# Kernel tuning notes

Measured on AMD Instinct MI355X. Metric: run time of the kernel, lower is better.

The kernel has to match this reference:

```python
import jax, jax.numpy as jnp
import numpy as np

NUM_HEADS = 16


def setup_inputs() -> dict:
    key = jax.random.key(0)
    ks = jax.random.split(key, 8)
    B, S, E = 2, 2048, 1024
    std = 0.02
    return {
        "q": jax.random.normal(ks[0], (B, S, E), dtype=jnp.float32),
        "k": jax.random.normal(ks[1], (B, S, E), dtype=jnp.float32),
        "v": jax.random.normal(ks[2], (B, S, E), dtype=jnp.float32),
        "Wq": jax.random.normal(ks[3], (E, E), dtype=jnp.float32) * std,
        "Wk": jax.random.normal(ks[4], (E, E), dtype=jnp.float32) * std,
        "Wv": jax.random.normal(ks[5], (E, E), dtype=jnp.float32) * std,
        "Wo": jax.random.normal(ks[6], (E, E), dtype=jnp.float32) * std,
        "bo": jnp.zeros((E,), dtype=jnp.float32),
    }


def reference(q, k, v, Wq, Wk, Wv, Wo, bo):
    B, S, E = q.shape
    H = NUM_HEADS
    D = E // H
    # projections (nn.Linear: x @ W.T)
    Q = (q @ Wq.T).reshape(B, S, H, D).transpose(0, 2, 1, 3)  # [B,H,S,D]
    K = (k @ Wk.T).reshape(B, S, H, D).transpose(0, 2, 1, 3)
    V = (v @ Wv.T).reshape(B, S, H, D).transpose(0, 2, 1, 3)
    scores = jnp.einsum("bhsd,bhtd->bhst", Q, K)  # [B,H,S,S]
    # causal mask applied before scaling (as in source; -inf/sqrt(d) == -inf)
    causal = jnp.tril(jnp.ones((S, S), dtype=bool))
    scores = jnp.where(causal, scores, -jnp.inf)
    scores = scores / np.sqrt(D).astype(np.float32)
    attn = jax.nn.softmax(scores, axis=-1)
    out = jnp.einsum("bhst,bhtd->bhsd", attn, V)  # [B,H,S,D]
    out = out.transpose(0, 2, 1, 3).reshape(B, S, E)
    return out @ Wo.T + bo
```

## Files before the change

kernel.cpp:

```cpp
#include <hip/hip_runtime.h>

typedef unsigned short u16;
typedef __bf16 bf16x8 __attribute__((ext_vector_type(8)));
typedef float f32x4 __attribute__((ext_vector_type(4)));
typedef unsigned u32x4 __attribute__((ext_vector_type(4)));

#define B_ 2
#define S_ 2048
#define E_ 1024
#define H_ 16
#define D_ 64
#define M_ (B_ * S_)

__device__ inline u16 f2bf(float f) {
  union { float f; unsigned int u; } c; c.f = f;
  unsigned int u = c.u;
  return (u16)((u + 0x7FFFu + ((u >> 16) & 1u)) >> 16);
}

__device__ inline f32x4 mfma16(bf16x8 a, bf16x8 b, f32x4 c) {
  return __builtin_amdgcn_mfma_f32_16x16x32_bf16(a, b, c, 0, 0, 0);
}

__device__ inline void gload16(const void* g, void* lds) {
  __builtin_amdgcn_global_load_lds(
      (const __attribute__((address_space(1))) unsigned int*)g,
      (__attribute__((address_space(3))) unsigned int*)lds, 16, 0, 0);
}

struct CvtArgs {
  const float* src[7];
  u16* dst[7];
  int n[7];
};

__global__ __launch_bounds__(256) void cvt_kernel(CvtArgs a) {
  const int arr = blockIdx.y;
  const int n = a.n[arr];
  const float* __restrict__ s = a.src[arr];
  u16* __restrict__ d = a.dst[arr];
  const int stride = gridDim.x * blockDim.x;
  for (int i = blockIdx.x * blockDim.x + threadIdx.x; i * 4 < n; i += stride) {
    const float4 f = *(const float4*)(s + 4 * i);
    ushort4 o;
    o.x = f2bf(f.x); o.y = f2bf(f.y); o.z = f2bf(f.z); o.w = f2bf(f.w);
    *(ushort4*)(d + 4 * i) = o;
  }
}

__global__ __launch_bounds__(256, 3) void qkv_gemm(
    const u16* __restrict__ qb, const u16* __restrict__ kb,
    const u16* __restrict__ vbp, const u16* __restrict__ Wqb,
    const u16* __restrict__ Wkb, const u16* __restrict__ Wvb,
    u16* __restrict__ Qh, u16* __restrict__ Kh, u16* __restrict__ Vt) {
  constexpr int BM = 128, BN = 128, BK = 32;
  __shared__ alignas(16) u16 As[3][BM * BK];
  __shared__ alignas(16) u16 Bs[3][BN * BK];

  const int wg = blockIdx.x;
  const int xcd = wg & 7, idx = wg >> 3;
  const int nb = idx & 7, mz = idx >> 3;
  const int z = mz >> 2;
  const int m0 = (xcd * 4 + (mz & 3)) * BM, n0 = nb * BN;

  const u16* A  = (z == 0) ? qb  : (z == 1) ? kb  : vbp;
  const u16* Bt = (z == 0) ? Wqb : (z == 1) ? Wkb : Wvb;
  u16* outp     = (z == 0) ? Qh  : (z == 1) ? Kh  : Vt;

  const int tid = threadIdx.x;
  const int wave = tid >> 6, lane = tid & 63;
  const int wm = (wave >> 1) * 64, wn = (wave & 1) * 64;
  const int fr = lane & 15, fc = lane >> 4;
  const int lrow = lane >> 2;
  const int lcol_sw = (((lane & 3) ^ ((lrow >> 1) & 3)) * 8);

  f32x4 acc[4][4] = {};

  u16 *aA = As[0], *aB = As[1], *aC = As[2];
  u16 *bA = Bs[0], *bB = Bs[1], *bC = Bs[2];

  auto stage = [&](int k0, u16* as, u16* bs) {
#pragma unroll
    for (int i = 0; i < 2; ++i) {
      const int chunk = wave * 2 + i;
      const int row = chunk * 16 + lrow;
      gload16(A + (size_t)(m0 + row) * E_ + k0 + lcol_sw, as + chunk * 16 * BK);
      gload16(Bt + (size_t)(n0 + row) * E_ + k0 + lcol_sw, bs + chunk * 16 * BK);
    }
  };

  constexpr int NK = E_ / BK;
  stage(0, aA, bA);
  stage(BK, aB, bB);

  const int sl = (fc ^ ((fr >> 1) & 3)) * 8;

  for (int t = 0; t < NK; ++t) {
    if (t + 1 < NK) {
      asm volatile("s_waitcnt vmcnt(4)" ::: "memory");
    } else {
      asm volatile("s_waitcnt vmcnt(0)" ::: "memory");
    }
    __builtin_amdgcn_s_barrier();
    __builtin_amdgcn_sched_barrier(0);

    if (t + 2 < NK) stage((t + 2) * BK, aC, bC);

    bf16x8 af[4], bfr[4];
#pragma unroll
    for (int mi = 0; mi < 4; ++mi)
      af[mi] = *(const bf16x8*)&aA[(wm + mi * 16 + fr) * BK + sl];
#pragma unroll
    for (int ni = 0; ni < 4; ++ni)
      bfr[ni] = *(const bf16x8*)&bA[(wn + ni * 16 + fr) * BK + sl];
    __builtin_amdgcn_s_setprio(1);
#pragma unroll
    for (int mi = 0; mi < 4; ++mi)
#pragma unroll
      for (int ni = 0; ni < 4; ++ni)
        acc[mi][ni] = mfma16(af[mi], bfr[ni], acc[mi][ni]);
    __builtin_amdgcn_s_setprio(0);

    u16* tp;
    tp = aA; aA = aB; aB = aC; aC = tp;
    tp = bA; bA = bB; bB = bC; bC = tp;
  }

#pragma unroll
  for (int mi = 0; mi < 4; ++mi)
#pragma unroll
    for (int ni = 0; ni < 4; ++ni)
#pragma unroll
      for (int r = 0; r < 4; ++r) {
        const int m = m0 + wm + mi * 16 + (fc << 2) + r;
        const int n = n0 + wn + ni * 16 + fr;
        const float v = acc[mi][ni][r];
        const int b = m >> 11, s = m & (S_ - 1), h = n >> 6, d = n & 63;
        if (z != 2) {
          outp[((((size_t)b * H_ + h) * S_ + s) << 6) + d] = f2bf(v);
        } else {
          outp[(((size_t)b * H_ + h) * D_ + d) * S_ + s] = f2bf(v);
        }
      }
}

__global__ __launch_bounds__(256, 4) void oproj_gemm(
    const u16* __restrict__ A, const u16* __restrict__ Bt,
    const float* __restrict__ bias, float* __restrict__ outp) {
  constexpr int BM = 64, BN = 128, BK = 32;
  __shared__ alignas(16) u16 As[3][BM * BK];
  __shared__ alignas(16) u16 Bs[3][BN * BK];

  const int wg = blockIdx.x;
  const int xcd = wg & 7, idx = wg >> 3;
  const int nb = idx & 7, mi_ = idx >> 3;
  const int m0 = (xcd * 8 + mi_) * BM, n0 = nb * BN;

  const int tid = threadIdx.x;
  const int wave = tid >> 6, lane = tid & 63;
  const int wm = (wave >> 1) * 32, wn = (wave & 1) * 64;
  const int fr = lane & 15, fc = lane >> 4;
  const int lrow = lane >> 2;
  const int lcol_sw = (((lane & 3) ^ ((lrow >> 1) & 3)) * 8);

  f32x4 acc[2][4] = {};

  u16 *aA = As[0], *aB = As[1], *aC = As[2];
  u16 *bA = Bs[0], *bB = Bs[1], *bC = Bs[2];

  auto stage = [&](int k0, u16* as, u16* bs) {
#pragma unroll
    for (int i = 0; i < 3; ++i) {
      const int c = wave + 4 * i;
      if (c < 4)
        gload16(A + (size_t)(m0 + c * 16 + lrow) * E_ + k0 + lcol_sw, as + c * 16 * BK);
      else
        gload16(Bt + (size_t)(n0 + (c - 4) * 16 + lrow) * E_ + k0 + lcol_sw,
                bs + (c - 4) * 16 * BK);
    }
  };

  constexpr int NK = E_ / BK;
  stage(0, aA, bA);
  stage(BK, aB, bB);

  const int sl = (fc ^ ((fr >> 1) & 3)) * 8;

  for (int t = 0; t < NK; ++t) {
    if (t + 1 < NK) {
      asm volatile("s_waitcnt vmcnt(3)" ::: "memory");
    } else {
      asm volatile("s_waitcnt vmcnt(0)" ::: "memory");
    }
    __builtin_amdgcn_s_barrier();
    __builtin_amdgcn_sched_barrier(0);

    if (t + 2 < NK) stage((t + 2) * BK, aC, bC);

    bf16x8 af[2], bfr[4];
#pragma unroll
    for (int mi = 0; mi < 2; ++mi)
      af[mi] = *(const bf16x8*)&aA[(wm + mi * 16 + fr) * BK + sl];
#pragma unroll
    for (int ni = 0; ni < 4; ++ni)
      bfr[ni] = *(const bf16x8*)&bA[(wn + ni * 16 + fr) * BK + sl];
    __builtin_amdgcn_s_setprio(1);
#pragma unroll
    for (int mi = 0; mi < 2; ++mi)
#pragma unroll
      for (int ni = 0; ni < 4; ++ni)
        acc[mi][ni] = mfma16(af[mi], bfr[ni], acc[mi][ni]);
    __builtin_amdgcn_s_setprio(0);

    u16* tp;
    tp = aA; aA = aB; aB = aC; aC = tp;
    tp = bA; bA = bB; bB = bC; bC = tp;
  }

#pragma unroll
  for (int mi = 0; mi < 2; ++mi)
#pragma unroll
    for (int ni = 0; ni < 4; ++ni)
#pragma unroll
      for (int r = 0; r < 4; ++r) {
        const int m = m0 + wm + mi * 16 + (fc << 2) + r;
        const int n = n0 + wn + ni * 16 + fr;
        outp[(size_t)m * E_ + n] = acc[mi][ni][r] + bias[n];
      }
}


__device__ __forceinline__ void stage_kv8(
    const u16* __restrict__ Kh_head, const u16* __restrict__ Vt_head,
    int kv0, u16* kb, u16* vb, int wq, int lane) {
  gload16(Kh_head + (size_t)(kv0 + lane) * D_ + wq * 8, kb + wq * 512);
  gload16(Vt_head + (size_t)lane * S_ + kv0 + wq * 8, vb + wq * 512);
}

__global__ __launch_bounds__(512, 4) void flash_attn(
    const u16* __restrict__ Qh, const u16* __restrict__ Kh,
    const u16* __restrict__ Vt, u16* __restrict__ O) {
  __shared__ alignas(16) u16 Kb[3][4096];
  __shared__ alignas(16) u16 Vb[3][4096];

  const int i = blockIdx.x;
  const int ch = i >> 8, p = i & 255;
  const int j = (ch << 8) + ((ch & 1) ? (255 - p) : p);
  const int qt = 15 - (j >> 5);
  const int bh = j & 31;

  const int tid = threadIdx.x;
  const int wq = tid >> 6, lane = tid & 63;

  const int q0 = qt * 128;
  const int b = bh >> 4, h = bh & 15;
  constexpr float SC = 0.125f * 1.4426950408889634f;
  const int fr = lane & 15, fc = lane >> 4;

  const u16* Qbase = Qh + ((size_t)bh * S_ + q0 + wq * 16 + fr) * D_ + 8 * fc;
  const bf16x8 qf0 = *(const bf16x8*)Qbase;
  const bf16x8 qf1 = *(const bf16x8*)(Qbase + 32);
  const u16* Kh_head = Kh + (size_t)bh * S_ * D_;
  const u16* Vt_head = Vt + (size_t)bh * D_ * S_;

  float lacc = 0.f;
  f32x4 oacc[4] = {};
  const int nt = 2 * qt + 2;

  u16 *kA = Kb[0], *kB = Kb[1], *kC = Kb[2];
  u16 *vA = Vb[0], *vB = Vb[1], *vC = Vb[2];

  stage_kv8(Kh_head, Vt_head, 0, kA, vA, wq, lane);
  stage_kv8(Kh_head, Vt_head, 64, kB, vB, wq, lane);

  for (int t = 0; t < nt; ++t) {
    if (t + 1 < nt) {
      asm volatile("s_waitcnt vmcnt(2)" ::: "memory");
    } else {
      asm volatile("s_waitcnt vmcnt(0)" ::: "memory");
    }
    __builtin_amdgcn_s_barrier();
    __builtin_amdgcn_sched_barrier(0);

    if (t + 2 < nt)
      stage_kv8(Kh_head, Vt_head, (t + 2) * 64, kC, vC, wq, lane);

    const u16* kb = kA;
    const u16* vb = vA;

    f32x4 sacc[4] = {};
    __builtin_amdgcn_s_setprio(1);
#pragma unroll
    for (int ni = 0; ni < 4; ++ni) {
      const bf16x8 k0 = *(const bf16x8*)&kb[fc * 512 + (16 * ni + fr) * 8];
      const bf16x8 k1 = *(const bf16x8*)&kb[(fc + 4) * 512 + (16 * ni + fr) * 8];
      sacc[ni] = mfma16(k0, qf0, sacc[ni]);
      sacc[ni] = mfma16(k1, qf1, sacc[ni]);
    }
    __builtin_amdgcn_s_setprio(0);

    const bool diag = (t >= nt - 2);
    const int qg = q0 + wq * 16 + fr;
    const int kvb = t * 64;
#pragma unroll
    for (int ni = 0; ni < 4; ++ni)
#pragma unroll
      for (int r = 0; r < 4; ++r) {
        const int kvg = kvb + 16 * ni + 4 * fc + r;
        float pv;
        if (diag && kvg > qg) {
          pv = 0.f;
        } else {
          pv = __builtin_amdgcn_exp2f(sacc[ni][r] * SC);
        }
        sacc[ni][r] = pv;
        lacc += pv;
      }

    unsigned w[4][2];
#pragma unroll
    for (int ni = 0; ni < 4; ++ni) {
      asm("v_cvt_pk_bf16_f32 %0, %1, %2"
          : "=v"(w[ni][0]) : "v"(sacc[ni][0]), "v"(sacc[ni][1]));
      asm("v_cvt_pk_bf16_f32 %0, %1, %2"
          : "=v"(w[ni][1]) : "v"(sacc[ni][2]), "v"(sacc[ni][3]));
    }

    unsigned paw0[4], paw1[4];
#pragma unroll
    for (int pair = 0; pair < 2; ++pair) {
      unsigned xx[2], yy[2], tt[2];
#pragma unroll
      for (int hh = 0; hh < 2; ++hh) {
        unsigned a = w[2 * pair][hh], bb = w[2 * pair + 1][hh];
        asm volatile("v_permlane32_swap_b32 %0, %1" : "+v"(a), "+v"(bb));
        xx[hh] = a; yy[hh] = bb;
        const unsigned s = (fc & 1) ? a : bb;
        tt[hh] = (unsigned)__shfl_xor((int)s, 16);
      }
      unsigned* pw_ = pair ? paw1 : paw0;
      pw_[0] = (fc & 1) ? tt[0] : xx[0];
      pw_[1] = (fc & 1) ? tt[1] : xx[1];
      pw_[2] = (fc & 1) ? yy[0] : tt[0];
      pw_[3] = (fc & 1) ? yy[1] : tt[1];
    }
    bf16x8 pa0, pa1;
    {
      u32x4 t0 = {paw0[0], paw0[1], paw0[2], paw0[3]};
      u32x4 t1 = {paw1[0], paw1[1], paw1[2], paw1[3]};
      __builtin_memcpy(&pa0, &t0, 16);
      __builtin_memcpy(&pa1, &t1, 16);
    }

    __builtin_amdgcn_s_setprio(1);
#pragma unroll
    for (int nd = 0; nd < 4; ++nd) {
      const bf16x8 v0 = *(const bf16x8*)&vb[fc * 512 + (16 * nd + fr) * 8];
      const bf16x8 v1 = *(const bf16x8*)&vb[(fc + 4) * 512 + (16 * nd + fr) * 8];
      oacc[nd] = mfma16(pa0, v0, oacc[nd]);
      oacc[nd] = mfma16(pa1, v1, oacc[nd]);
    }
    __builtin_amdgcn_s_setprio(0);

    u16* tk = kA; kA = kB; kB = kC; kC = tk;
    u16* tv = vA; vA = vB; vB = vC; vC = tv;
  }

  float l = lacc;
  l += __shfl_xor(l, 16);
  l += __shfl_xor(l, 32);
  float linv[4];
#pragma unroll
  for (int r = 0; r < 4; ++r)
    linv[r] = __builtin_amdgcn_rcpf(__shfl(l, 4 * fc + r));

#pragma unroll
  for (int nd = 0; nd < 4; ++nd) {
#pragma unroll
    for (int r = 0; r < 4; ++r) {
      const int qr = q0 + wq * 16 + (fc << 2) + r;
      const int d = 16 * nd + fr;
      const float v = oacc[nd][r] * linv[r];
      O[((size_t)b * S_ + qr) * E_ + h * D_ + d] = f2bf(v);
    }
  }
}

extern "C" void kernel_launch(void* const* d_in, const int* in_sizes, int n_in,
                              void* d_out, int out_size, void* d_ws, size_t ws_size,
                              hipStream_t stream) {
  const float* q  = (const float*)d_in[0];
  const float* k  = (const float*)d_in[1];
  const float* v  = (const float*)d_in[2];
  const float* Wq = (const float*)d_in[3];
  const float* Wk = (const float*)d_in[4];
  const float* Wv = (const float*)d_in[5];
  const float* Wo = (const float*)d_in[6];
  const float* bo = (const float*)d_in[7];

  const size_t nBSE = (size_t)M_ * E_;
  const size_t nEE  = (size_t)E_ * E_;
  u16* qb  = (u16*)d_ws;
  u16* kb  = qb + nBSE;
  u16* vb  = kb + nBSE;
  u16* Wqb = vb + nBSE;
  u16* Wkb = Wqb + nEE;
  u16* Wvb = Wkb + nEE;
  u16* Wob = Wvb + nEE;
  u16* Qh  = Wob + nEE;
  u16* Kh  = Qh + nBSE;
  u16* Vt  = qb;
  u16* Oa  = vb;

  CvtArgs ca;
  ca.src[0] = q;  ca.dst[0] = qb;  ca.n[0] = (int)nBSE;
  ca.src[1] = k;  ca.dst[1] = kb;  ca.n[1] = (int)nBSE;
  ca.src[2] = v;  ca.dst[2] = vb;  ca.n[2] = (int)nBSE;
  ca.src[3] = Wq; ca.dst[3] = Wqb; ca.n[3] = (int)nEE;
  ca.src[4] = Wk; ca.dst[4] = Wkb; ca.n[4] = (int)nEE;
  ca.src[5] = Wv; ca.dst[5] = Wvb; ca.n[5] = (int)nEE;
  ca.src[6] = Wo; ca.dst[6] = Wob; ca.n[6] = (int)nEE;
  cvt_kernel<<<dim3(512, 7), 256, 0, stream>>>(ca);

  qkv_gemm<<<dim3(768), 256, 0, stream>>>(
      qb, kb, vb, Wqb, Wkb, Wvb, Qh, Kh, Vt);
  flash_attn<<<dim3(512), 512, 0, stream>>>(Qh, Kh, Vt, Oa);
  oproj_gemm<<<dim3(512), 256, 0, stream>>>(Oa, Wob, bo, (float*)d_out);
}
```

Before: 115.5 us.

## Fuse fp32-to-bf16 activation conversion into QKV GEMM A-tile loading

The QKV projection GEMM now reads the fp32 q/k/v activations directly into registers, converts them to bf16 with packed convert instructions, and writes them swizzled into LDS. The separate conversion pass over the three large activation tensors is dropped, so the conversion kernel only handles the weights. This removes one full write and reread of the activations through global memory. In exchange, A-tile loads go through registers rather than direct global-to-LDS loads, adding register pressure, extra LDS write instructions and an lgkmcnt wait each iteration.

```diff
diff --git a/kernel.cpp b/kernel.cpp
--- a/kernel.cpp
+++ b/kernel.cpp
@@ -29,9 +29,9 @@
 }
 
 struct CvtArgs {
-  const float* src[7];
-  u16* dst[7];
-  int n[7];
+  const float* src[4];
+  u16* dst[4];
+  int n[4];
 };
 
 __global__ __launch_bounds__(256) void cvt_kernel(CvtArgs a) {
@@ -49,8 +49,8 @@
 }
 
 __global__ __launch_bounds__(256, 3) void qkv_gemm(
-    const u16* __restrict__ qb, const u16* __restrict__ kb,
-    const u16* __restrict__ vbp, const u16* __restrict__ Wqb,
+    const float* __restrict__ qf, const float* __restrict__ kf,
+    const float* __restrict__ vf, const u16* __restrict__ Wqb,
     const u16* __restrict__ Wkb, const u16* __restrict__ Wvb,
     u16* __restrict__ Qh, u16* __restrict__ Kh, u16* __restrict__ Vt) {
   constexpr int BM = 128, BN = 128, BK = 32;
@@ -63,9 +63,9 @@
   const int z = mz >> 2;
   const int m0 = (xcd * 4 + (mz & 3)) * BM, n0 = nb * BN;
 
-  const u16* A  = (z == 0) ? qb  : (z == 1) ? kb  : vbp;
-  const u16* Bt = (z == 0) ? Wqb : (z == 1) ? Wkb : Wvb;
-  u16* outp     = (z == 0) ? Qh  : (z == 1) ? Kh  : Vt;
+  const float* A = (z == 0) ? qf  : (z == 1) ? kf  : vf;
+  const u16* Bt  = (z == 0) ? Wqb : (z == 1) ? Wkb : Wvb;
+  u16* outp      = (z == 0) ? Qh  : (z == 1) ? Kh  : Vt;
 
   const int tid = threadIdx.x;
   const int wave = tid >> 6, lane = tid & 63;
@@ -74,37 +74,77 @@
   const int lrow = lane >> 2;
   const int lcol_sw = (((lane & 3) ^ ((lrow >> 1) & 3)) * 8);
 
+  const int arow_sub = lane >> 3;
+  const int acol = (lane & 7) * 4;
+  const int a_chunkbase = wave * 2;
+
   f32x4 acc[4][4] = {};
 
   u16 *aA = As[0], *aB = As[1], *aC = As[2];
   u16 *bA = Bs[0], *bB = Bs[1], *bC = Bs[2];
 
-  auto stage = [&](int k0, u16* as, u16* bs) {
+  float4 areg[4];
+
+  auto loadA = [&](int k0) {
+#pragma unroll
+    for (int ci = 0; ci < 2; ++ci)
+#pragma unroll
+      for (int i2 = 0; i2 < 2; ++i2) {
+        const int row = (a_chunkbase + ci) * 16 + i2 * 8 + arow_sub;
+        areg[ci * 2 + i2] = *(const float4*)(A + (size_t)(m0 + row) * E_ + k0 + acol);
+      }
+  };
+  auto writeA = [&](u16* as) {
+#pragma unroll
+    for (int ci = 0; ci < 2; ++ci)
+#pragma unroll
+      for (int i2 = 0; i2 < 2; ++i2) {
+        const int rowLoc = i2 * 8 + arow_sub;
+        const int row = (a_chunkbase + ci) * 16 + rowLoc;
+        const float4 f = areg[ci * 2 + i2];
+        unsigned d0, d1;
+        asm("v_cvt_pk_bf16_f32 %0, %1, %2" : "=v"(d0) : "v"(f.x), "v"(f.y));
+        asm("v_cvt_pk_bf16_f32 %0, %1, %2" : "=v"(d1) : "v"(f.z), "v"(f.w));
+        const int slot = (acol >> 3) ^ ((rowLoc >> 1) & 3);
+        const int half = (acol >> 2) & 1;
+        *(uint2*)(&as[row * 32 + slot * 8 + half * 4]) = make_uint2(d0, d1);
+      }
+  };
+  auto loadB = [&](int k0, u16* bs) {
 #pragma unroll
     for (int i = 0; i < 2; ++i) {
       const int chunk = wave * 2 + i;
       const int row = chunk * 16 + lrow;
-      gload16(A + (size_t)(m0 + row) * E_ + k0 + lcol_sw, as + chunk * 16 * BK);
       gload16(Bt + (size_t)(n0 + row) * E_ + k0 + lcol_sw, bs + chunk * 16 * BK);
     }
   };
 
   constexpr int NK = E_ / BK;
-  stage(0, aA, bA);
-  stage(BK, aB, bB);
+  loadA(0);
+  loadB(0, bA);
+  asm volatile("s_waitcnt vmcnt(2)" ::: "memory");
+  writeA(aA);
+  loadA(BK);
+  loadB(BK, bB);
 
   const int sl = (fc ^ ((fr >> 1) & 3)) * 8;
 
   for (int t = 0; t < NK; ++t) {
     if (t + 1 < NK) {
-      asm volatile("s_waitcnt vmcnt(4)" ::: "memory");
+      asm volatile("s_waitcnt vmcnt(2)" ::: "memory");
+      writeA(aB);
     } else {
       asm volatile("s_waitcnt vmcnt(0)" ::: "memory");
     }
+    asm volatile("s_waitcnt lgkmcnt(0)" ::: "memory");
     __builtin_amdgcn_s_barrier();
     __builtin_amdgcn_sched_barrier(0);
 
-    if (t + 2 < NK) stage((t + 2) * BK, aC, bC);
+    if (t + 2 < NK) {
+      loadA((t + 2) * BK);
+      loadB((t + 2) * BK, bC);
+    }
+    __builtin_amdgcn_sched_barrier(0);
 
     bf16x8 af[4], bfr[4];
 #pragma unroll
@@ -228,7 +268,6 @@
         outp[(size_t)m * E_ + n] = acc[mi][ni][r] + bias[n];
       }
 }
-
 
 __device__ __forceinline__ void stage_kv8(
     const u16* __restrict__ Kh_head, const u16* __restrict__ Vt_head,
@@ -400,30 +439,24 @@
 
   const size_t nBSE = (size_t)M_ * E_;
   const size_t nEE  = (size_t)E_ * E_;
-  u16* qb  = (u16*)d_ws;
-  u16* kb  = qb + nBSE;
-  u16* vb  = kb + nBSE;
-  u16* Wqb = vb + nBSE;
+  u16* Wqb = (u16*)d_ws;
   u16* Wkb = Wqb + nEE;
   u16* Wvb = Wkb + nEE;
   u16* Wob = Wvb + nEE;
   u16* Qh  = Wob + nEE;
   u16* Kh  = Qh + nBSE;
-  u16* Vt  = qb;
-  u16* Oa  = vb;
+  u16* Vt  = Kh + nBSE;
+  u16* Oa  = Vt + nBSE;
 
   CvtArgs ca;
-  ca.src[0] = q;  ca.dst[0] = qb;  ca.n[0] = (int)nBSE;
-  ca.src[1] = k;  ca.dst[1] = kb;  ca.n[1] = (int)nBSE;
-  ca.src[2] = v;  ca.dst[2] = vb;  ca.n[2] = (int)nBSE;
-  ca.src[3] = Wq; ca.dst[3] = Wqb; ca.n[3] = (int)nEE;
-  ca.src[4] = Wk; ca.dst[4] = Wkb; ca.n[4] = (int)nEE;
-  ca.src[5] = Wv; ca.dst[5] = Wvb; ca.n[5] = (int)nEE;
-  ca.src[6] = Wo; ca.dst[6] = Wob; ca.n[6] = (int)nEE;
-  cvt_kernel<<<dim3(512, 7), 256, 0, stream>>>(ca);
+  ca.src[0] = Wq; ca.dst[0] = Wqb; ca.n[0] = (int)nEE;
+  ca.src[1] = Wk; ca.dst[1] = Wkb; ca.n[1] = (int)nEE;
+  ca.src[2] = Wv; ca.dst[2] = Wvb; ca.n[2] = (int)nEE;
+  ca.src[3] = Wo; ca.dst[3] = Wob; ca.n[3] = (int)nEE;
+  cvt_kernel<<<dim3(256, 4), 256, 0, stream>>>(ca);
 
   qkv_gemm<<<dim3(768), 256, 0, stream>>>(
-      qb, kb, vb, Wqb, Wkb, Wvb, Qh, Kh, Vt);
+      q, k, v, Wqb, Wkb, Wvb, Qh, Kh, Vt);
   flash_attn<<<dim3(512), 512, 0, stream>>>(Qh, Kh, Vt, Oa);
   oproj_gemm<<<dim3(512), 256, 0, stream>>>(Oa, Wob, bo, (float*)d_out);
 }
```

Measured after the change: 111.5 us. 1.04x faster.
